# Kernel tuning notes

Measured on AMD Instinct MI355X. Metric: run time of the kernel, lower is better.

The kernel has to match this reference:

```python
import jax, jax.numpy as jnp
import numpy as np
from jax import lax

N, G, L, D, E, STEPS = 65536, 128, 512, 128, 262144, 6
C = 2 * D  # concat dim (input_dim + output_dim)


def setup_inputs() -> dict:
    key = jax.random.key(0)
    ks = jax.random.split(key, 12)
    sD = 1.0 / float(np.sqrt(D))
    sC = 1.0 / float(np.sqrt(C))
    return {
        "x": jax.random.normal(ks[0], (N, D), jnp.float32),
        "edge_index": jax.random.randint(ks[1], (2, E), 0, N, dtype=jnp.int32),
        "edge_weight": jax.random.uniform(ks[2], (E,), jnp.float32),
        "batch": (jnp.arange(N) // L).astype(jnp.int32),  # sorted graph ids, L nodes/graph
        "ggnn_w": jax.random.normal(ks[3], (STEPS, D, D), jnp.float32) * sD,
        "gru_wih": jax.random.normal(ks[4], (3 * D, D), jnp.float32) * sD,
        "gru_whh": jax.random.normal(ks[5], (3 * D, D), jnp.float32) * sD,
        "gru_bih": jnp.zeros((3 * D,), jnp.float32),
        "gru_bhh": jnp.zeros((3 * D,), jnp.float32),
        "conv1_w": jax.random.normal(ks[6], (D, D, 3), jnp.float32) * sD,
        "conv1_b": jnp.zeros((D,), jnp.float32),
        "conv2_w": jax.random.normal(ks[7], (D, D, 1), jnp.float32) * sD,
        "conv2_b": jnp.zeros((D,), jnp.float32),
        "convc1_w": jax.random.normal(ks[8], (C, C, 3), jnp.float32) * sC,
        "convc1_b": jnp.zeros((C,), jnp.float32),
        "convc2_w": jax.random.normal(ks[9], (C, C, 1), jnp.float32) * sC,
        "convc2_b": jnp.zeros((C,), jnp.float32),
        "bn1_g": jnp.ones((D,), jnp.float32),
        "bn1_b": jnp.zeros((D,), jnp.float32),
        "bn2_g": jnp.ones((C,), jnp.float32),
        "bn2_b": jnp.zeros((C,), jnp.float32),
        "mlpy_w": jax.random.normal(ks[10], (2, D), jnp.float32) * sD,
        "mlpy_b": jnp.zeros((2,), jnp.float32),
        "mlpz_w": jax.random.normal(ks[11], (2, C), jnp.float32) * sC,
        "mlpz_b": jnp.zeros((2,), jnp.float32),
    }


def _gru(m, h, wih, whh, bih, bhh):
    gx = m @ wih.T + bih
    gh = h @ whh.T + bhh
    xr, xz, xn = jnp.split(gx, 3, axis=-1)
    hr, hz, hn = jnp.split(gh, 3, axis=-1)
    r = jax.nn.sigmoid(xr + hr)
    z = jax.nn.sigmoid(xz + hz)
    n = jnp.tanh(xn + r * hn)
    return (1.0 - z) * n + z * h


def _conv1d(x, w, b):  # x [G,Cin,L], w [Cout,Cin,K]
    y = lax.conv_general_dilated(x, w, (1,), "VALID", dimension_numbers=("NCH", "OIH", "NCH"))
    return y + b[None, :, None]


def _maxpool(x, k, s):
    return lax.reduce_window(x, -jnp.inf, lax.max, (1, 1, k), (1, 1, s), "VALID")


def _bn(x, g, b):  # training-mode BatchNorm1d over (N, L) per channel
    mean = x.mean(axis=(0, 2), keepdims=True)
    var = x.var(axis=(0, 2), keepdims=True)
    return (x - mean) * lax.rsqrt(var + 1e-5) * g[None, :, None] + b[None, :, None]


def reference(x, edge_index, edge_weight, batch, ggnn_w, gru_wih, gru_whh, gru_bih,
              gru_bhh, conv1_w, conv1_b, conv2_w, conv2_b, convc1_w, convc1_b,
              convc2_w, convc2_b, bn1_g, bn1_b, bn2_g, bn2_b, mlpy_w, mlpy_b,
              mlpz_w, mlpz_b):
    src, dst = edge_index[0], edge_index[1]

    # GatedGraphConv: per layer linear -> weighted message scatter-add -> GRU update
    def step(h, w):
        m = h @ w
        agg = jax.ops.segment_sum(m[src] * edge_weight[:, None], dst, num_segments=N)
        return _gru(agg, h, gru_wih, gru_whh, gru_bih, gru_bhh), None

    h, _ = lax.scan(step, x, ggnn_w)

    # de_batchify_graphs: one fused scatter into zero-padded [G, L, *] tensor
    counts = jax.ops.segment_sum(jnp.ones((N,), jnp.int32), batch, num_segments=G)
    offsets = jnp.cumsum(counts) - counts
    pos = jnp.arange(N) - offsets[batch]
    x_i = jnp.zeros((G, L, D), x.dtype).at[batch, pos].set(x)
    h_i = jnp.zeros((G, L, D), h.dtype).at[batch, pos].set(h)
    c_i = jnp.concatenate([h_i, x_i], axis=-1)  # [G, L, 2D]

    hT = h_i.transpose(0, 2, 1)  # [G, D, L]
    Y1 = _maxpool(jax.nn.relu(_bn(_conv1d(hT, conv1_w, conv1_b), bn1_g, bn1_b)), 3, 2)
    Y2 = _maxpool(jax.nn.relu(_bn(_conv1d(Y1, conv2_w, conv2_b), bn1_g, bn1_b)), 2, 2).transpose(0, 2, 1)
    cT = c_i.transpose(0, 2, 1)  # [G, 2D, L]
    Z1 = _maxpool(jax.nn.relu(_bn(_conv1d(cT, convc1_w, convc1_b), bn2_g, bn2_b)), 3, 2)
    Z2 = _maxpool(jax.nn.relu(_bn(_conv1d(Z1, convc2_w, convc2_b), bn2_g, bn2_b)), 2, 2).transpose(0, 2, 1)

    before_avg = (Y2 @ mlpy_w.T + mlpy_b) * (Z2 @ mlpz_w.T + mlpz_b)  # [G, L', 2]
    return before_avg.mean(axis=1)  # [G, 2]
```

## Files before the change

### kernel.cpp

```cpp
#include <hip/hip_runtime.h>
#include <math.h>

#define NN 65536
#define GG 128
#define LL 512
#define DD 128
#define EE 262144
#define NSTEPS 6
#define CC 256
#define L1 510
#define P1 254
#define P2 127

typedef __attribute__((ext_vector_type(8))) short s8bf;
typedef __attribute__((ext_vector_type(4))) float f4acc;

__device__ __forceinline__ unsigned short f2bf(float x) {
  unsigned u = __float_as_uint(x);
  unsigned r = u + 0x7FFFu + ((u >> 16) & 1u);
  return (unsigned short)(r >> 16);
}
__device__ __forceinline__ float bf2f(unsigned short h) {
  return __uint_as_float(((unsigned)h) << 16);
}
__device__ __forceinline__ unsigned short f2bf_sel(float x, int lo_sel) {
  unsigned short hi = f2bf(x);
  if (!lo_sel) return hi;
  return f2bf(x - bf2f(hi));
}
__device__ __forceinline__ uint2 pack4bf(float4 v, int lo_sel) {
  unsigned short s0 = f2bf_sel(v.x, lo_sel), s1 = f2bf_sel(v.y, lo_sel);
  unsigned short s2 = f2bf_sel(v.z, lo_sel), s3 = f2bf_sel(v.w, lo_sel);
  uint2 pk; pk.x = (unsigned)s0 | ((unsigned)s1 << 16);
  pk.y = (unsigned)s2 | ((unsigned)s3 << 16);
  return pk;
}

__global__ __launch_bounds__(256) void k_prep(
    const float* __restrict__ wih, const float* __restrict__ whh,
    const float* __restrict__ gw,
    const float* __restrict__ w1, const float* __restrict__ wc1,
    const float* __restrict__ w2, const float* __restrict__ wc2,
    unsigned short* __restrict__ wihCh, unsigned short* __restrict__ wihCl,
    unsigned short* __restrict__ whhCh, unsigned short* __restrict__ whhCl,
    unsigned short* __restrict__ gwTh, unsigned short* __restrict__ gwTl,
    unsigned short* __restrict__ c1h, unsigned short* __restrict__ c1l,
    unsigned short* __restrict__ cc1h, unsigned short* __restrict__ cc1l,
    unsigned short* __restrict__ c2h, unsigned short* __restrict__ c2l,
    unsigned short* __restrict__ cc2h, unsigned short* __restrict__ cc2l) {
  int i = blockIdx.x * 256 + threadIdx.x;
  if (i < 49152) {
    float v = wih[i];
    unsigned short h_ = f2bf(v);
    wihCh[i] = h_; wihCl[i] = f2bf(v - bf2f(h_));
    float u = whh[i];
    unsigned short h2 = f2bf(u);
    whhCh[i] = h2; whhCl[i] = f2bf(u - bf2f(h2));
  }
  if (i < 98304) {
    int s = i >> 14; int r = i & 16383; int c = r >> 7; int k = r & 127;
    float v = gw[(s << 14) + k * 128 + c];
    unsigned short h_ = f2bf(v);
    gwTh[i] = h_; gwTl[i] = f2bf(v - bf2f(h_));
  }
  if (i < 49152) {
    int ci = i & 127; int r = i >> 7; int co = r & 127; int tap = r >> 7;
    float v = w1[(co * 128 + ci) * 3 + tap];
    unsigned short h_ = f2bf(v);
    c1h[i] = h_; c1l[i] = f2bf(v - bf2f(h_));
  }
  if (i < 196608) {
    int ci = i & 255; int r = i >> 8; int co = r & 255; int tap = r >> 8;
    float v = wc1[(co * 256 + ci) * 3 + tap];
    unsigned short h_ = f2bf(v);
    cc1h[i] = h_; cc1l[i] = f2bf(v - bf2f(h_));
  }
  if (i < 16384) {
    float v = w2[i];
    unsigned short h_ = f2bf(v);
    c2h[i] = h_; c2l[i] = f2bf(v - bf2f(h_));
  }
  if (i < 65536) {
    float v = wc2[i];
    unsigned short h_ = f2bf(v);
    cc2h[i] = h_; cc2l[i] = f2bf(v - bf2f(h_));
  }
}

__global__ __launch_bounds__(256) void k_xsplit(const float* __restrict__ src,
                                                unsigned short* __restrict__ dh,
                                                unsigned short* __restrict__ dl) {
  int i = (blockIdx.x * 256 + threadIdx.x) * 4;
  float4 v = *(const float4*)&src[i];
  unsigned short hx = f2bf(v.x), hy = f2bf(v.y), hz = f2bf(v.z), hw = f2bf(v.w);
  uint2 hp; hp.x = (unsigned)hx | ((unsigned)hy << 16);
  hp.y = (unsigned)hz | ((unsigned)hw << 16);
  *(uint2*)&dh[i] = hp;
  unsigned short lx = f2bf(v.x - bf2f(hx)), ly = f2bf(v.y - bf2f(hy));
  unsigned short lz = f2bf(v.z - bf2f(hz)), lw = f2bf(v.w - bf2f(hw));
  uint2 lp; lp.x = (unsigned)lx | ((unsigned)ly << 16);
  lp.y = (unsigned)lz | ((unsigned)lw << 16);
  *(uint2*)&dl[i] = lp;
}

__global__ __launch_bounds__(256) void k_hist(const int* __restrict__ dst, int* __restrict__ cnt) {
  int e = blockIdx.x * 256 + threadIdx.x;
  if (e < EE) atomicAdd(&cnt[dst[e]], 1);
}

__global__ __launch_bounds__(1024) void k_scan(const int* __restrict__ cnt,
                                               int* __restrict__ rowptr,
                                               int* __restrict__ cursor) {
  __shared__ int part[1024];
  int t = threadIdx.x;
  int base = t * 64;
  int s = 0;
  for (int i = 0; i < 64; i++) s += cnt[base + i];
  part[t] = s;
  __syncthreads();
  for (int off = 1; off < 1024; off <<= 1) {
    int v = part[t];
    int u = (t >= off) ? part[t - off] : 0;
    __syncthreads();
    part[t] = v + u;
    __syncthreads();
  }
  int run = part[t] - s;
  for (int i = 0; i < 64; i++) {
    rowptr[base + i] = run;
    cursor[base + i] = run;
    run += cnt[base + i];
  }
  if (t == 1023) rowptr[NN] = run;
}

__global__ __launch_bounds__(256) void k_fill(const int* __restrict__ src,
                                              const int* __restrict__ dst,
                                              const float* __restrict__ ew,
                                              int* __restrict__ cursor,
                                              int* __restrict__ col,
                                              float* __restrict__ wgt) {
  int e = blockIdx.x * 256 + threadIdx.x;
  if (e < EE) {
    int d = dst[e];
    int p = atomicAdd(&cursor[d], 1);
    col[p] = src[e];
    wgt[p] = ew[e];
  }
}

__global__ __launch_bounds__(256, 4) void k_gemm_mfma(
    const float* __restrict__ A,
    const unsigned short* __restrict__ Wh, const unsigned short* __restrict__ Wl,
    float* __restrict__ Cout) {
  __shared__ __attribute__((aligned(16))) unsigned short As[64 * 136];
  int t = threadIdx.x;
  int r0 = blockIdx.x * 64;
  int wv = t >> 6, lane = t & 63;
  int ln = lane & 15, q = lane >> 4;
  f4acc acc[4][2];
#pragma unroll
  for (int mt = 0; mt < 4; mt++)
#pragma unroll
    for (int nt = 0; nt < 2; nt++) acc[mt][nt] = (f4acc)0.f;

  for (int p = 0; p < 3; p++) {
    if (p != 1) {
      const int a_lo = (p == 2);
      if (p) __syncthreads();
      for (int base = t * 4; base < 64 * 128; base += 1024) {
        int row = base >> 7, kk = base & 127;
        float4 v = *(const float4*)&A[(r0 + row) * 128 + kk];
        *(uint2*)&As[row * 136 + kk] = pack4bf(v, a_lo);
      }
      __syncthreads();
    }
    const unsigned short* W = (p == 1) ? Wl : Wh;
#pragma unroll
    for (int k0 = 0; k0 < 128; k0 += 32) {
      s8bf af[4], bf[2];
#pragma unroll
      for (int nt = 0; nt < 2; nt++)
        bf[nt] = *(const s8bf*)&W[(wv * 32 + nt * 16 + ln) * 128 + k0 + q * 8];
#pragma unroll
      for (int mt = 0; mt < 4; mt++)
        af[mt] = *(const s8bf*)&As[(mt * 16 + ln) * 136 + k0 + q * 8];
#pragma unroll
      for (int mt = 0; mt < 4; mt++)
#pragma unroll
        for (int nt = 0; nt < 2; nt++)
          acc[mt][nt] = __builtin_amdgcn_mfma_f32_16x16x32_bf16(af[mt], bf[nt], acc[mt][nt], 0, 0, 0);
    }
  }
#pragma unroll
  for (int mt = 0; mt < 4; mt++)
#pragma unroll
    for (int nt = 0; nt < 2; nt++)
#pragma unroll
      for (int reg = 0; reg < 4; reg++) {
        int r = r0 + mt * 16 + q * 4 + reg;
        Cout[r * 128 + wv * 32 + nt * 16 + ln] = acc[mt][nt][reg];
      }
}

__global__ __launch_bounds__(256) void k_gather(const float* __restrict__ m,
                                                const int* __restrict__ rowptr,
                                                const int* __restrict__ col,
                                                const float* __restrict__ wgt,
                                                float* __restrict__ agg) {
  int t = threadIdx.x;
  int n = blockIdx.x * 8 + (t >> 5);
  int c4 = t & 31;
  const float4* m4 = (const float4*)m;
  int s0 = rowptr[n], s1 = rowptr[n + 1];
  float ax = 0.f, ay = 0.f, az = 0.f, aw = 0.f;
  int e = s0;
  for (; e + 2 <= s1; e += 2) {
    int cA = col[e], cB = col[e + 1];
    float wA = wgt[e], wB = wgt[e + 1];
    float4 vA = m4[cA * 32 + c4];
    float4 vB = m4[cB * 32 + c4];
    ax += vA.x * wA + vB.x * wB;
    ay += vA.y * wA + vB.y * wB;
    az += vA.z * wA + vB.z * wB;
    aw += vA.w * wA + vB.w * wB;
  }
  if (e < s1) {
    int cA = col[e];
    float wA = wgt[e];
    float4 vA = m4[cA * 32 + c4];
    ax += vA.x * wA; ay += vA.y * wA; az += vA.z * wA; aw += vA.w * wA;
  }
  ((float4*)agg)[n * 32 + c4] = make_float4(ax, ay, az, aw);
}

__global__ __launch_bounds__(256, 2) void k_gru_mfma(
    const float* __restrict__ agg, const float* __restrict__ hin,
    const unsigned short* __restrict__ wihCh, const unsigned short* __restrict__ wihCl,
    const unsigned short* __restrict__ whhCh, const unsigned short* __restrict__ whhCl,
    const float* __restrict__ bih, const float* __restrict__ bhh,
    float* __restrict__ hout) {
  __shared__ __attribute__((aligned(16))) unsigned short As[2 * 64 * 136];
  int t = threadIdx.x;
  int r0 = blockIdx.x * 64;
  int d0 = blockIdx.y * 64;
  int wv = t >> 6, lane = t & 63;
  int ln = lane & 15, q = lane >> 4;
  f4acc acc[4][6];
#pragma unroll
  for (int mt = 0; mt < 4; mt++)
#pragma unroll
    for (int tg = 0; tg < 6; tg++) acc[mt][tg] = (f4acc)0.f;

  for (int p = 0; p < 3; p++) {
    if (p != 1) {
      const int a_lo = (p == 2);
      if (p) __syncthreads();
#pragma unroll
      for (int mat = 0; mat < 2; mat++) {
        const float* Asrc = mat ? hin : agg;
        for (int base = t * 4; base < 64 * 128; base += 1024) {
          int row = base >> 7, kk = base & 127;
          float4 v = *(const float4*)&Asrc[(r0 + row) * 128 + kk];
          *(uint2*)&As[mat * 8704 + row * 136 + kk] = pack4bf(v, a_lo);
        }
      }
      __syncthreads();
    }
    const unsigned short* wx = (p == 1) ? wihCl : wihCh;
    const unsigned short* wh = (p == 1) ? whhCl : whhCh;
#pragma unroll
    for (int k0 = 0; k0 < 128; k0 += 32) {
      s8bf af[2][4], bfr[6];
#pragma unroll
      for (int tg = 0; tg < 6; tg++) {
        int gate = (tg < 3) ? tg : tg - 3;
        const unsigned short* W = (tg < 3) ? wx : wh;
        bfr[tg] = *(const s8bf*)&W[(gate * 128 + d0 + wv * 16 + ln) * 128 + k0 + q * 8];
      }
#pragma unroll
      for (int mat = 0; mat < 2; mat++)
#pragma unroll
        for (int mt = 0; mt < 4; mt++)
          af[mat][mt] = *(const s8bf*)&As[mat * 8704 + (mt * 16 + ln) * 136 + k0 + q * 8];
#pragma unroll
      for (int mt = 0; mt < 4; mt++)
#pragma unroll
        for (int tg = 0; tg < 6; tg++)
          acc[mt][tg] = __builtin_amdgcn_mfma_f32_16x16x32_bf16(
              af[tg < 3 ? 0 : 1][mt], bfr[tg], acc[mt][tg], 0, 0, 0);
    }
  }
  int d = d0 + wv * 16 + ln;
  float bi0 = bih[d], bi1 = bih[128 + d], bi2 = bih[256 + d];
  float bh0 = bhh[d], bh1 = bhh[128 + d], bh2 = bhh[256 + d];
#pragma unroll
  for (int mt = 0; mt < 4; mt++) {
#pragma unroll
    for (int reg = 0; reg < 4; reg++) {
      int r = r0 + mt * 16 + q * 4 + reg;
      float hold = hin[r * 128 + d];
      float xr = acc[mt][0][reg] + bi0;
      float xz = acc[mt][1][reg] + bi1;
      float xn = acc[mt][2][reg] + bi2;
      float hr = acc[mt][3][reg] + bh0;
      float hz = acc[mt][4][reg] + bh1;
      float hn = acc[mt][5][reg] + bh2;
      float rr = 1.f / (1.f + expf(-(xr + hr)));
      float zz = 1.f / (1.f + expf(-(xz + hz)));
      float nnv = tanhf(xn + rr * hn);
      hout[r * 128 + d] = (1.f - zz) * nnv + zz * hold;
    }
  }
}

template<int CIN, int TAPS, int WA>
__global__ __launch_bounds__(256, 4) void k_conv_mfma(
    const unsigned short* __restrict__ inAh, const unsigned short* __restrict__ inAl,
    const unsigned short* __restrict__ inBh, const unsigned short* __restrict__ inBl,
    const unsigned short* __restrict__ Wh, const unsigned short* __restrict__ Wl,
    const float* __restrict__ bias, float* __restrict__ out,
    float* __restrict__ stats, int Lin, int Lco) {
  constexpr int APAD = CIN + 8;
  constexpr int ROWS = 64 + TAPS - 1;
  constexpr int NCH = CIN / 32;
  __shared__ __attribute__((aligned(16))) unsigned short As[ROWS * APAD];
  __shared__ float sred[256];
  const int g = blockIdx.z, co0 = blockIdx.y * 128, l0 = blockIdx.x * 64;
  const int t = threadIdx.x;
  const int wv = t >> 6, lane = t & 63, ln = lane & 15, q = lane >> 4;
  f4acc acc[4][2];
#pragma unroll
  for (int mt = 0; mt < 4; mt++)
#pragma unroll
    for (int nt = 0; nt < 2; nt++) acc[mt][nt] = (f4acc)0.f;

  for (int p = 0; p < 3; p++) {
    if (p != 1) {
      const unsigned short* pA = (p == 2) ? inAl : inAh;
      const unsigned short* pB = (p == 2) ? inBl : inBh;
      if (p) __syncthreads();
      for (int base = t * 8; base < ROWS * CIN; base += 2048) {
        int row = base / CIN, ch = base % CIN;
        int lr = l0 + row; if (lr > Lin - 1) lr = Lin - 1;
        uint4 v;
        if (ch < WA) v = *(const uint4*)&pA[(g * Lin + lr) * WA + ch];
        else         v = *(const uint4*)&pB[(g * Lin + lr) * WA + ch - WA];
        *(uint4*)&As[row * APAD + ch] = v;
      }
      __syncthreads();
    }
    const unsigned short* W = (p == 1) ? Wl : Wh;
#pragma unroll
    for (int tap = 0; tap < TAPS; tap++) {
#pragma unroll
      for (int ch = 0; ch < NCH; ch++) {
        const int c0 = ch * 32;
        s8bf af[4], bf[2];
#pragma unroll
        for (int nt = 0; nt < 2; nt++)
          bf[nt] = *(const s8bf*)&W[(tap * CIN + co0 + wv * 32 + nt * 16 + ln) * CIN + c0 + q * 8];
#pragma unroll
        for (int mt = 0; mt < 4; mt++)
          af[mt] = *(const s8bf*)&As[(mt * 16 + ln + tap) * APAD + c0 + q * 8];
#pragma unroll
        for (int mt = 0; mt < 4; mt++)
#pragma unroll
          for (int nt = 0; nt < 2; nt++)
            acc[mt][nt] = __builtin_amdgcn_mfma_f32_16x16x32_bf16(af[mt], bf[nt], acc[mt][nt], 0, 0, 0);
      }
    }
  }
  sred[t] = 0.f;
  __syncthreads();
#pragma unroll
  for (int nt = 0; nt < 2; nt++) {
    int cl = wv * 32 + nt * 16 + ln;
    int co = co0 + cl;
    float bv = bias[co];
    float s = 0.f, s2 = 0.f;
#pragma unroll
    for (int mt = 0; mt < 4; mt++)
#pragma unroll
      for (int reg = 0; reg < 4; reg++) {
        int l = l0 + mt * 16 + q * 4 + reg;
        if (l < Lco) {
          float v = acc[mt][nt][reg] + bv;
          out[(g * Lco + l) * CIN + co] = v;
          s += v; s2 += v * v;
        }
      }
    atomicAdd(&sred[cl], s);
    atomicAdd(&sred[128 + cl], s2);
  }
  __syncthreads();
  if (t < 128) atomicAdd(&stats[co0 + t], sred[t]);
  else atomicAdd(&stats[CIN + co0 + (t - 128)], sred[t]);
}

__global__ __launch_bounds__(256) void k_bnpool(const float* __restrict__ in,
                                                float* __restrict__ outF,
                                                unsigned short* __restrict__ outH,
                                                unsigned short* __restrict__ outL,
                                                const float* __restrict__ stats,
                                                const float* __restrict__ gamma,
                                                const float* __restrict__ beta,
                                                int Cch, int LinC, int Lout, int pk) {
  int idx = blockIdx.x * 256 + threadIdx.x;
  int total = GG * Cch * Lout;
  if (idx >= total) return;
  int c = idx & (Cch - 1);
  int r = idx / Cch;
  int p = r % Lout;
  int g = r / Lout;
  float cntf = (float)(GG * LinC);
  float mean = stats[c] / cntf;
  float var = stats[Cch + c] / cntf - mean * mean;
  float inv = rsqrtf(var + 1e-5f) * gamma[c];
  float sh = beta[c] - mean * inv;
  const float* base = &in[((g * LinC) + 2 * p) * Cch + c];
  float m = 0.f;
  for (int k = 0; k < pk; k++) {
    float v = fmaxf(base[k * Cch] * inv + sh, 0.f);
    m = fmaxf(m, v);
  }
  int oidx = (g * Lout + p) * Cch + c;
  if (outH) {
    unsigned short hi = f2bf(m);
    outH[oidx] = hi;
    outL[oidx] = f2bf(m - bf2f(hi));
  } else {
    outF[oidx] = m;
  }
}

__global__ __launch_bounds__(128) void k_final(const float* __restrict__ Y2,
                                               const float* __restrict__ Z2,
                                               const float* __restrict__ myw,
                                               const float* __restrict__ myb,
                                               const float* __restrict__ mzw,
                                               const float* __restrict__ mzb,
                                               float* __restrict__ outp) {
  __shared__ float red0[128];
  __shared__ float red1[128];
  int g = blockIdx.x;
  int t = threadIdx.x;
  float y0 = myb[0], y1 = myb[1], z0 = mzb[0], z1 = mzb[1];
  if (t < P2) {
    const float* yb = &Y2[(g * P2 + t) * 128];
    for (int c = 0; c < 128; c++) {
      float v = yb[c];
      y0 += v * myw[c];
      y1 += v * myw[128 + c];
    }
    const float* zb = &Z2[(g * P2 + t) * 256];
    for (int c = 0; c < 256; c++) {
      float v = zb[c];
      z0 += v * mzw[c];
      z1 += v * mzw[256 + c];
    }
  }
  red0[t] = (t < P2) ? y0 * z0 : 0.f;
  red1[t] = (t < P2) ? y1 * z1 : 0.f;
  __syncthreads();
  for (int off = 64; off > 0; off >>= 1) {
    if (t < off) {
      red0[t] += red0[t + off];
      red1[t] += red1[t + off];
    }
    __syncthreads();
  }
  if (t == 0) {
    outp[g * 2 + 0] = red0[0] / 127.f;
    outp[g * 2 + 1] = red1[0] / 127.f;
  }
}

extern "C" void kernel_launch(void* const* d_in, const int* in_sizes, int n_in,
                              void* d_out, int out_size, void* d_ws, size_t ws_size,
                              hipStream_t stream) {
  const float* x   = (const float*)d_in[0];
  const int* ei    = (const int*)d_in[1];
  const float* ew  = (const float*)d_in[2];
  const float* gw  = (const float*)d_in[4];
  const float* wih = (const float*)d_in[5];
  const float* whh = (const float*)d_in[6];
  const float* bih = (const float*)d_in[7];
  const float* bhh = (const float*)d_in[8];
  const float* w1  = (const float*)d_in[9];
  const float* b1  = (const float*)d_in[10];
  const float* w2  = (const float*)d_in[11];
  const float* b2  = (const float*)d_in[12];
  const float* wc1 = (const float*)d_in[13];
  const float* bc1 = (const float*)d_in[14];
  const float* wc2 = (const float*)d_in[15];
  const float* bc2 = (const float*)d_in[16];
  const float* bn1g = (const float*)d_in[17];
  const float* bn1b = (const float*)d_in[18];
  const float* bn2g = (const float*)d_in[19];
  const float* bn2b = (const float*)d_in[20];
  const float* myw = (const float*)d_in[21];
  const float* myb = (const float*)d_in[22];
  const float* mzw = (const float*)d_in[23];
  const float* mzb = (const float*)d_in[24];
  float* out = (float*)d_out;

  float* ws    = (float*)d_ws;
  float* slotP = ws;
  float* bufA  = slotP + 8388608;
  float* bufB  = bufA + 16711680;
  float* bufC  = bufB + 8388608;
  float* Y2    = bufC + 8388608;
  float* Z2    = Y2 + 2080768;
  float* wslot = Z2 + 4161536;
  unsigned short* wihCh = (unsigned short*)wslot;
  unsigned short* wihCl = wihCh + 49152;
  unsigned short* whhCh = wihCl + 49152;
  unsigned short* whhCl = whhCh + 49152;
  unsigned short* c1h  = (unsigned short*)(wslot + 98304);
  unsigned short* c1l  = c1h + 49152;
  unsigned short* cc1h = c1l + 49152;
  unsigned short* cc1l = cc1h + 196608;
  unsigned short* c2h  = cc1l + 196608;
  unsigned short* c2l  = c2h + 16384;
  unsigned short* cc2h = c2l + 16384;
  unsigned short* cc2l = cc2h + 65536;
  float* stats = (float*)(cc2l + 65536);
  int* cnt    = (int*)(stats + 512);
  int* rowptr = cnt + 65536;
  int* cursor = rowptr + 65537;
  int* col    = cursor + 65536;
  float* wgt  = (float*)(col + 262144);
  unsigned short* gwTh = (unsigned short*)(wgt + 262144);
  unsigned short* gwTl = gwTh + 98304;
  size_t needed = (size_t)((float*)(gwTl + 98304) - ws) * 4;
  if (ws_size < needed) return;

  float* P = slotP;
  float* Q = bufC;
  float* m = bufA;
  float* agg = bufB;
  unsigned short* hPh = (unsigned short*)bufB;
  unsigned short* hPl = hPh + 8388608;
  unsigned short* xPh = (unsigned short*)bufC;
  unsigned short* xPl = xPh + 8388608;
  unsigned short* p1h = (unsigned short*)bufC;
  unsigned short* p1l = p1h + 8323072;
  float* convOut = bufA;
  float* c2out = bufA;

  const int* src = ei;
  const int* dst = ei + EE;

  k_prep<<<768, 256, 0, stream>>>(wih, whh, gw, w1, wc1, w2, wc2,
                                  wihCh, wihCl, whhCh, whhCl, gwTh, gwTl,
                                  c1h, c1l, cc1h, cc1l, c2h, c2l, cc2h, cc2l);
  hipMemsetAsync(cnt, 0, 65536 * 4, stream);
  k_hist<<<1024, 256, 0, stream>>>(dst, cnt);
  k_scan<<<1, 1024, 0, stream>>>(cnt, rowptr, cursor);
  k_fill<<<1024, 256, 0, stream>>>(src, dst, ew, cursor, col, wgt);

  for (int s = 0; s < NSTEPS; s++) {
    const float* hcur = (s == 0) ? x : ((s & 1) ? Q : P);
    float* hnext = (s & 1) ? P : Q;
    k_gemm_mfma<<<1024, 256, 0, stream>>>(hcur, gwTh + s * 16384, gwTl + s * 16384, m);
    k_gather<<<8192, 256, 0, stream>>>(m, rowptr, col, wgt, agg);
    k_gru_mfma<<<dim3(1024, 2), 256, 0, stream>>>(agg, hcur, wihCh, wihCl,
                                                  whhCh, whhCl, bih, bhh, hnext);
  }

  k_xsplit<<<8192, 256, 0, stream>>>(P, hPh, hPl);
  k_xsplit<<<8192, 256, 0, stream>>>(x, xPh, xPl);

  hipMemsetAsync(stats, 0, 512 * 4, stream);
  k_conv_mfma<256, 3, 128><<<dim3(8, 2, 128), 256, 0, stream>>>(
      hPh, hPl, xPh, xPl, cc1h, cc1l, bc1, convOut, stats, 512, L1);
  k_bnpool<<<(GG * 256 * P1 + 255) / 256, 256, 0, stream>>>(
      convOut, nullptr, p1h, p1l, stats, bn2g, bn2b, 256, L1, P1, 3);
  hipMemsetAsync(stats, 0, 512 * 4, stream);
  k_conv_mfma<256, 1, 256><<<dim3(4, 2, 128), 256, 0, stream>>>(
      p1h, p1l, nullptr, nullptr, cc2h, cc2l, bc2, c2out, stats, P1, P1);
  k_bnpool<<<(GG * 256 * P2 + 255) / 256, 256, 0, stream>>>(
      c2out, Z2, nullptr, nullptr, stats, bn2g, bn2b, 256, P1, P2, 2);

  hipMemsetAsync(stats, 0, 512 * 4, stream);
  k_conv_mfma<128, 3, 128><<<dim3(8, 1, 128), 256, 0, stream>>>(
      hPh, hPl, nullptr, nullptr, c1h, c1l, b1, convOut, stats, 512, L1);
  k_bnpool<<<(GG * 128 * P1 + 255) / 256, 256, 0, stream>>>(
      convOut, nullptr, p1h, p1l, stats, bn1g, bn1b, 128, L1, P1, 3);
  hipMemsetAsync(stats, 0, 512 * 4, stream);
  k_conv_mfma<128, 1, 128><<<dim3(4, 1, 128), 256, 0, stream>>>(
      p1h, p1l, nullptr, nullptr, c2h, c2l, b2, c2out, stats, P1, P1);
  k_bnpool<<<(GG * 128 * P2 + 255) / 256, 256, 0, stream>>>(
      c2out, Y2, nullptr, nullptr, stats, bn1g, bn1b, 128, P1, P2, 2);

  k_final<<<128, 128, 0, stream>>>(Y2, Z2, myw, myb, mzw, mzb, out);
}
```

Baseline: 1.676 ms.

## Stage both bf16 halves once in GEMM, unroll gather, merge memsets

New measurement: 1.725 ms. 1.03x slower.

```diff
diff --git a/kernel.cpp b/kernel.cpp
--- a/kernel.cpp
+++ b/kernel.cpp
@@ -34,6 +34,17 @@
   uint2 pk; pk.x = (unsigned)s0 | ((unsigned)s1 << 16);
   pk.y = (unsigned)s2 | ((unsigned)s3 << 16);
   return pk;
+}
+__device__ __forceinline__ void pack4bf_both(float4 v, uint2* hi_out, uint2* lo_out) {
+  unsigned short hx = f2bf(v.x), hy = f2bf(v.y), hz = f2bf(v.z), hw = f2bf(v.w);
+  uint2 hp; hp.x = (unsigned)hx | ((unsigned)hy << 16);
+  hp.y = (unsigned)hz | ((unsigned)hw << 16);
+  *hi_out = hp;
+  unsigned short lx = f2bf(v.x - bf2f(hx)), ly = f2bf(v.y - bf2f(hy));
+  unsigned short lz = f2bf(v.z - bf2f(hz)), lw = f2bf(v.w - bf2f(hw));
+  uint2 lp; lp.x = (unsigned)lx | ((unsigned)ly << 16);
+  lp.y = (unsigned)lz | ((unsigned)lw << 16);
+  *lo_out = lp;
 }
 
 __global__ __launch_bounds__(256) void k_prep(
@@ -92,14 +103,9 @@
                                                 unsigned short* __restrict__ dl) {
   int i = (blockIdx.x * 256 + threadIdx.x) * 4;
   float4 v = *(const float4*)&src[i];
-  unsigned short hx = f2bf(v.x), hy = f2bf(v.y), hz = f2bf(v.z), hw = f2bf(v.w);
-  uint2 hp; hp.x = (unsigned)hx | ((unsigned)hy << 16);
-  hp.y = (unsigned)hz | ((unsigned)hw << 16);
+  uint2 hp, lp;
+  pack4bf_both(v, &hp, &lp);
   *(uint2*)&dh[i] = hp;
-  unsigned short lx = f2bf(v.x - bf2f(hx)), ly = f2bf(v.y - bf2f(hy));
-  unsigned short lz = f2bf(v.z - bf2f(hz)), lw = f2bf(v.w - bf2f(hw));
-  uint2 lp; lp.x = (unsigned)lx | ((unsigned)ly << 16);
-  lp.y = (unsigned)lz | ((unsigned)lw << 16);
   *(uint2*)&dl[i] = lp;
 }
 
@@ -153,7 +159,7 @@
     const float* __restrict__ A,
     const unsigned short* __restrict__ Wh, const unsigned short* __restrict__ Wl,
     float* __restrict__ Cout) {
-  __shared__ __attribute__((aligned(16))) unsigned short As[64 * 136];
+  __shared__ __attribute__((aligned(16))) unsigned short As[2 * 64 * 136];
   int t = threadIdx.x;
   int r0 = blockIdx.x * 64;
   int wv = t >> 6, lane = t & 63;
@@ -164,17 +170,18 @@
 #pragma unroll
     for (int nt = 0; nt < 2; nt++) acc[mt][nt] = (f4acc)0.f;
 
+  for (int base = t * 4; base < 64 * 128; base += 1024) {
+    int row = base >> 7, kk = base & 127;
+    float4 v = *(const float4*)&A[(r0 + row) * 128 + kk];
+    uint2 hp, lp;
+    pack4bf_both(v, &hp, &lp);
+    *(uint2*)&As[row * 136 + kk] = hp;
+    *(uint2*)&As[8704 + row * 136 + kk] = lp;
+  }
+  __syncthreads();
+
   for (int p = 0; p < 3; p++) {
-    if (p != 1) {
-      const int a_lo = (p == 2);
-      if (p) __syncthreads();
-      for (int base = t * 4; base < 64 * 128; base += 1024) {
-        int row = base >> 7, kk = base & 127;
-        float4 v = *(const float4*)&A[(r0 + row) * 128 + kk];
-        *(uint2*)&As[row * 136 + kk] = pack4bf(v, a_lo);
-      }
-      __syncthreads();
-    }
+    const int abase = (p == 2) ? 8704 : 0;
     const unsigned short* W = (p == 1) ? Wl : Wh;
 #pragma unroll
     for (int k0 = 0; k0 < 128; k0 += 32) {
@@ -184,7 +191,7 @@
         bf[nt] = *(const s8bf*)&W[(wv * 32 + nt * 16 + ln) * 128 + k0 + q * 8];
 #pragma unroll
       for (int mt = 0; mt < 4; mt++)
-        af[mt] = *(const s8bf*)&As[(mt * 16 + ln) * 136 + k0 + q * 8];
+        af[mt] = *(const s8bf*)&As[abase + (mt * 16 + ln) * 136 + k0 + q * 8];
 #pragma unroll
       for (int mt = 0; mt < 4; mt++)
 #pragma unroll
@@ -214,27 +221,31 @@
   const float4* m4 = (const float4*)m;
   int s0 = rowptr[n], s1 = rowptr[n + 1];
   float ax = 0.f, ay = 0.f, az = 0.f, aw = 0.f;
-  int e = s0;
-  for (; e + 2 <= s1; e += 2) {
-    int cA = col[e], cB = col[e + 1];
-    float wA = wgt[e], wB = wgt[e + 1];
-    float4 vA = m4[cA * 32 + c4];
-    float4 vB = m4[cB * 32 + c4];
-    ax += vA.x * wA + vB.x * wB;
-    ay += vA.y * wA + vB.y * wB;
-    az += vA.z * wA + vB.z * wB;
-    aw += vA.w * wA + vB.w * wB;
-  }
-  if (e < s1) {
-    int cA = col[e];
-    float wA = wgt[e];
-    float4 vA = m4[cA * 32 + c4];
-    ax += vA.x * wA; ay += vA.y * wA; az += vA.z * wA; aw += vA.w * wA;
+  int cc[8];
+  float ww[8];
+#pragma unroll
+  for (int i = 0; i < 8; i++) {
+    int e = s0 + i;
+    int ec = (e < EE) ? e : (EE - 1);
+    cc[i] = col[ec];
+    ww[i] = (e < s1) ? wgt[ec] : 0.f;
+  }
+#pragma unroll
+  for (int i = 0; i < 8; i++) {
+    float4 v = m4[cc[i] * 32 + c4];
+    ax += v.x * ww[i]; ay += v.y * ww[i];
+    az += v.z * ww[i]; aw += v.w * ww[i];
+  }
+  for (int e = s0 + 8; e < s1; e++) {
+    int c = col[e];
+    float w = wgt[e];
+    float4 v = m4[c * 32 + c4];
+    ax += v.x * w; ay += v.y * w; az += v.z * w; aw += v.w * w;
   }
   ((float4*)agg)[n * 32 + c4] = make_float4(ax, ay, az, aw);
 }
 
-__global__ __launch_bounds__(256, 2) void k_gru_mfma(
+__global__ __launch_bounds__(256, 3) void k_gru_mfma(
     const float* __restrict__ agg, const float* __restrict__ hin,
     const unsigned short* __restrict__ wihCh, const unsigned short* __restrict__ wihCl,
     const unsigned short* __restrict__ whhCh, const unsigned short* __restrict__ whhCl,
@@ -526,7 +537,7 @@
   unsigned short* cc2h = c2l + 16384;
   unsigned short* cc2l = cc2h + 65536;
   float* stats = (float*)(cc2l + 65536);
-  int* cnt    = (int*)(stats + 512);
+  int* cnt    = (int*)(stats + 2048);
   int* rowptr = cnt + 65536;
   int* cursor = rowptr + 65537;
   int* col    = cursor + 65536;
@@ -535,6 +546,11 @@
   unsigned short* gwTl = gwTh + 98304;
   size_t needed = (size_t)((float*)(gwTl + 98304) - ws) * 4;
   if (ws_size < needed) return;
+
+  float* statsZ1 = stats;
+  float* statsZ2 = stats + 512;
+  float* statsY1 = stats + 1024;
+  float* statsY2 = stats + 1536;
 
   float* P = slotP;
   float* Q = bufC;
@@ -555,7 +571,7 @@
   k_prep<<<768, 256, 0, stream>>>(wih, whh, gw, w1, wc1, w2, wc2,
                                   wihCh, wihCl, whhCh, whhCl, gwTh, gwTl,
                                   c1h, c1l, cc1h, cc1l, c2h, c2l, cc2h, cc2l);
-  hipMemsetAsync(cnt, 0, 65536 * 4, stream);
+  hipMemsetAsync(stats, 0, (2048 + 65536) * 4, stream);
   k_hist<<<1024, 256, 0, stream>>>(dst, cnt);
   k_scan<<<1, 1024, 0, stream>>>(cnt, rowptr, cursor);
   k_fill<<<1024, 256, 0, stream>>>(src, dst, ew, cursor, col, wgt);
@@ -572,27 +588,23 @@
   k_xsplit<<<8192, 256, 0, stream>>>(P, hPh, hPl);
   k_xsplit<<<8192, 256, 0, stream>>>(x, xPh, xPl);
 
-  hipMemsetAsync(stats, 0, 512 * 4, stream);
   k_conv_mfma<256, 3, 128><<<dim3(8, 2, 128), 256, 0, stream>>>(
-      hPh, hPl, xPh, xPl, cc1h, cc1l, bc1, convOut, stats, 512, L1);
+      hPh, hPl, xPh, xPl, cc1h, cc1l, bc1, convOut, statsZ1, 512, L1);
   k_bnpool<<<(GG * 256 * P1 + 255) / 256, 256, 0, stream>>>(
-      convOut, nullptr, p1h, p1l, stats, bn2g, bn2b, 256, L1, P1, 3);
-  hipMemsetAsync(stats, 0, 512 * 4, stream);
+      convOut, nullptr, p1h, p1l, statsZ1, bn2g, bn2b, 256, L1, P1, 3);
   k_conv_mfma<256, 1, 256><<<dim3(4, 2, 128), 256, 0, stream>>>(
-      p1h, p1l, nullptr, nullptr, cc2h, cc2l, bc2, c2out, stats, P1, P1);
+      p1h, p1l, nullptr, nullptr, cc2h, cc2l, bc2, c2out, statsZ2, P1, P1);
   k_bnpool<<<(GG * 256 * P2 + 255) / 256, 256, 0, stream>>>(
-      c2out, Z2, nullptr, nullptr, stats, bn2g, bn2b, 256, P1, P2, 2);
-
-  hipMemsetAsync(stats, 0, 512 * 4, stream);
+      c2out, Z2, nullptr, nullptr, statsZ2, bn2g, bn2b, 256, P1, P2, 2);
+
   k_conv_mfma<128, 3, 128><<<dim3(8, 1, 128), 256, 0, stream>>>(
-      hPh, hPl, nullptr, nullptr, c1h, c1l, b1, convOut, stats, 512, L1);
+      hPh, hPl, nullptr, nullptr, c1h, c1l, b1, convOut, statsY1, 512, L1);
   k_bnpool<<<(GG * 128 * P1 + 255) / 256, 256, 0, stream>>>(
-      convOut, nullptr, p1h, p1l, stats, bn1g, bn1b, 128, L1, P1, 3);
-  hipMemsetAsync(stats, 0, 512 * 4, stream);
+      convOut, nullptr, p1h, p1l, statsY1, bn1g, bn1b, 128, L1, P1, 3);
   k_conv_mfma<128, 1, 128><<<dim3(4, 1, 128), 256, 0, stream>>>(
-      p1h, p1l, nullptr, nullptr, c2h, c2l, b2, c2out, stats, P1, P1);
+      p1h, p1l, nullptr, nullptr, c2h, c2l, b2, c2out, statsY2, P1, P1);
   k_bnpool<<<(GG * 128 * P2 + 255) / 256, 256, 0, stream>>>(
-      c2out, Y2, nullptr, nullptr, stats, bn1g, bn1b, 128, P1, P2, 2);
+      c2out, Y2, nullptr, nullptr, statsY2, bn1g, bn1b, 128, P1, P2, 2);
 
   k_final<<<128, 128, 0, stream>>>(Y2, Z2, myw, myb, mzw, mzb, out);
 }
```
